# Performance work log

Hardware: AMD Instinct MI355X
Metric: run time of the kernel (lower is better)

Reference implementation:

```python
import jax, jax.numpy as jnp
import numpy as np


def setup_inputs() -> dict:
    key = jax.random.key(0)
    k1, k2, k3, k4, k5 = jax.random.split(key, 5)
    B, H, W, C = 4, 64, 64, 512
    ratio = 8
    d = C // ratio  # 64
    x = jax.random.normal(k1, (B, H, W, C), dtype=jnp.float32)
    # 1x1 conv weights (no bias) == channel-mixing matrices, he_normal-ish scale
    Wq = jax.random.normal(k2, (C, d), dtype=jnp.float32) * np.sqrt(2.0 / C)
    Wk = jax.random.normal(k3, (C, d), dtype=jnp.float32) * np.sqrt(2.0 / C)
    Wv = jax.random.normal(k4, (C, C), dtype=jnp.float32) * np.sqrt(2.0 / C)
    gamma = jax.random.normal(k5, (1,), dtype=jnp.float32)
    return {"x": x, "Wq": Wq, "Wk": Wk, "Wv": Wv, "gamma": gamma}


def reference(x, Wq, Wk, Wv, gamma):
    B, H, W, C = x.shape
    N = H * W
    # 1x1 convs (no bias) are per-pixel channel matmuls
    q = jnp.einsum('bhwc,cd->bhwd', x, Wq).reshape(B, N, -1)  # [B,N,d]
    k = jnp.einsum('bhwc,cd->bhwd', x, Wk).reshape(B, N, -1)  # [B,N,d]
    v = jnp.einsum('bhwc,cd->bhwd', x, Wv).reshape(B, N, C)   # [B,N,C]
    # energy[b,i,j] = key_i . query_j  (batch_dot(key, query^T))
    energy = jnp.einsum('bid,bjd->bij', k, q)                 # [B,N,N]
    attn = jax.nn.softmax(energy, axis=-1)
    out = jnp.einsum('bij,bjc->bic', attn, v)                 # [B,N,C]
    out = out.reshape(B, H, W, C)
    return gamma * out
```

## Files before the change

### kernel.cpp

```cpp
#include <hip/hip_runtime.h>
#include <hip/hip_bf16.h>

typedef unsigned short u16;
typedef unsigned int   u32;
typedef __attribute__((ext_vector_type(8))) short short8;
typedef __attribute__((ext_vector_type(4))) float f32x4;
typedef __attribute__((ext_vector_type(4))) u16   u16x4;

#define MFMA16(a,b,c) __builtin_amdgcn_mfma_f32_16x16x32_bf16((a),(b),(c),0,0,0)

#define BATCH 4
#define NPIX  4096
#define CCH   512
#define DDIM  64
#define MFIX  64.0f

static __device__ __forceinline__ u16 f2bf(float f){
  __hip_bfloat16 h = __float2bfloat16(f);
  return __builtin_bit_cast(u16, h);
}
static __device__ __forceinline__ float bf2f(u16 u){
  __hip_bfloat16 h = __builtin_bit_cast(__hip_bfloat16, u);
  return __bfloat162float(h);
}

__global__ __launch_bounds__(256) void k_wconv(const f32x4* __restrict__ wv,
                                               u16x4* __restrict__ wvb){
  const int i = blockIdx.x*256 + threadIdx.x;
  #pragma unroll
  for (int it=0; it<4; ++it){
    int idx = i + it*16384;
    f32x4 v = wv[idx];
    u16x4 o;
    o[0]=f2bf(v[0]); o[1]=f2bf(v[1]); o[2]=f2bf(v[2]); o[3]=f2bf(v[3]);
    wvb[idx] = o;
  }
}

__global__ __launch_bounds__(256) void k_qkproj(const float* __restrict__ x,
                                                const float* __restrict__ Wq,
                                                const float* __restrict__ Wk,
                                                u16* __restrict__ qhi, u16* __restrict__ qlo,
                                                u16* __restrict__ khi, u16* __restrict__ klo,
                                                u16* __restrict__ xhi){
  __shared__ float xs[32][512];
  const int pix0 = blockIdx.x * 32;
  {
    const f32x4* xg = (const f32x4*)(x + (size_t)pix0*CCH);
    f32x4* xsv = (f32x4*)(&xs[0][0]);
    #pragma unroll
    for (int it=0; it<16; ++it) xsv[threadIdx.x + it*256] = xg[threadIdx.x + it*256];
  }
  __syncthreads();
  #pragma unroll
  for (int e=0; e<16; ++e){
    int idx4 = e*256 + threadIdx.x;
    int f = idx4*4;
    int row = f >> 9, col = f & 511;
    f32x4 v = *(const f32x4*)(&xs[row][col]);
    u16x4 o;
    o[0]=f2bf(v[0]); o[1]=f2bf(v[1]); o[2]=f2bf(v[2]); o[3]=f2bf(v[3]);
    *(u16x4*)(&xhi[(size_t)(pix0+row)*CCH + col]) = o;
  }
  const int col = threadIdx.x & 127;
  const int grp = threadIdx.x >> 7;
  const float* W = (col < 64) ? Wq : Wk;
  const int wc = col & 63;
  float acc[16];
  #pragma unroll
  for (int p=0;p<16;++p) acc[p] = 0.f;
  #pragma unroll 2
  for (int c=0;c<512;c+=4){
    float w0 = W[(c+0)*64 + wc];
    float w1 = W[(c+1)*64 + wc];
    float w2 = W[(c+2)*64 + wc];
    float w3 = W[(c+3)*64 + wc];
    #pragma unroll
    for (int p=0;p<16;++p){
      f32x4 xv = *(const f32x4*)(&xs[grp*16+p][c]);
      acc[p] += xv[0]*w0 + xv[1]*w1 + xv[2]*w2 + xv[3]*w3;
    }
  }
  #pragma unroll
  for (int p=0;p<16;++p){
    int pix = pix0 + grp*16 + p;
    float v = acc[p];
    u16 hi = f2bf(v);
    u16 lo = f2bf(v - bf2f(hi));
    if (col < 64){ qhi[pix*64+wc] = hi; qlo[pix*64+wc] = lo; }
    else         { khi[pix*64+wc] = hi; klo[pix*64+wc] = lo; }
  }
}

__global__ __launch_bounds__(256) void k_vproj(const u16* __restrict__ xhi,
                                               const u16* __restrict__ wvb,
                                               u16* __restrict__ vJB){
  __shared__ u16 As[64][72];
  __shared__ u16 Bs[64][266];
  const int pix0 = blockIdx.x * 64;
  const int c0   = blockIdx.y * 256;
  const int tid = threadIdx.x;
  const int w = tid >> 6, l = tid & 63;
  const int lg = l >> 4, ll = l & 15;
  f32x4 acc[4][4];
  #pragma unroll
  for (int mf=0;mf<4;++mf)
    #pragma unroll
    for (int nf=0;nf<4;++nf){ f32x4 z = {0.f,0.f,0.f,0.f}; acc[mf][nf] = z; }

  for (int ks=0; ks<8; ++ks){
    __syncthreads();
    #pragma unroll
    for (int it=0; it<2; ++it){
      int ch = tid + it*256; int r = ch>>3, c8 = ch&7;
      *(uint4*)(&As[r][c8*8]) = *(const uint4*)(&xhi[(size_t)(pix0+r)*CCH + ks*64 + c8*8]);
    }
    #pragma unroll
    for (int it=0; it<8; ++it){
      int ch = tid + it*256; int r = ch>>5, c32 = ch&31;
      uint4 d = *(const uint4*)(&wvb[(size_t)(ks*64+r)*CCH + c0 + c32*8]);
      u32* dst = (u32*)(&Bs[r][c32*8]);
      dst[0]=d.x; dst[1]=d.y; dst[2]=d.z; dst[3]=d.w;
    }
    __syncthreads();
    #pragma unroll
    for (int kc=0;kc<2;++kc){
      short8 a[4];
      #pragma unroll
      for (int mf=0;mf<4;++mf) a[mf] = *(const short8*)(&As[mf*16 + ll][kc*32 + lg*8]);
      #pragma unroll
      for (int nf=0;nf<4;++nf){
        short8 bb;
        int cc = w*64 + nf*16 + ll;
        #pragma unroll
        for (int e=0;e<8;++e) bb[e] = (short)Bs[kc*32 + lg*8 + e][cc];
        #pragma unroll
        for (int mf=0;mf<4;++mf) acc[mf][nf] = MFMA16(a[mf], bb, acc[mf][nf]);
      }
    }
  }
  #pragma unroll
  for (int mf=0;mf<4;++mf){
    #pragma unroll
    for (int nf=0;nf<4;++nf){
      int pix = pix0 + mf*16 + lg*4;
      int c   = c0 + w*64 + nf*16 + ll;
      int bb  = pix >> 12;
      int j   = pix & 4095;
      u16x4 o;
      #pragma unroll
      for (int r=0;r<4;++r) o[r] = f2bf(acc[mf][nf][r]);
      size_t off = (((size_t)bb*64 + (j>>6))*CCH + c)*64 + (j&63);
      *(u16x4*)(vJB + off) = o;
    }
  }
}

__global__ __launch_bounds__(1024,4)
void k_attn(const u16* __restrict__ qhi, const u16* __restrict__ qlo,
            const u16* __restrict__ khi, const u16* __restrict__ klo,
            const u16* __restrict__ vJB, const float* __restrict__ gamma_p,
            float* __restrict__ out){
  __shared__ u16 Qs[2][2][64][76];
  __shared__ u16 Ps[2][64][76];
  __shared__ float l_part[16][16];
  __shared__ float l_s[64];
  const int bid = blockIdx.x;
  const int b  = bid & 3;
  const int i0 = (bid >> 2) * 64;
  const int tid = threadIdx.x;
  const int w = tid >> 6, l = tid & 63;
  const int lg = l >> 4, ll = l & 15;
  const int iw = (w & 3) * 16;
  const int jq = (w >> 2) * 16;
  const int cw = w * 32;

  const u16* qh_b  = qhi + (size_t)b*NPIX*DDIM;
  const u16* ql_b  = qlo + (size_t)b*NPIX*DDIM;
  const u16* vbase = vJB + (size_t)b*64*CCH*64;

  short8 kfh[2], kfl[2];
  #pragma unroll
  for (int kc=0;kc<2;++kc){
    size_t a = ((size_t)(b*NPIX + i0 + iw + ll))*DDIM + kc*32 + lg*8;
    kfh[kc] = *(const short8*)(khi + a);
    kfl[kc] = *(const short8*)(klo + a);
  }

  f32x4 acc[4][2];
  #pragma unroll
  for (int mf=0;mf<4;++mf)
    #pragma unroll
    for (int nf=0;nf<2;++nf){ f32x4 z = {0.f,0.f,0.f,0.f}; acc[mf][nf] = z; }
  float lsum = 0.f;

  const int spart = tid >> 9;
  const int srow  = (tid >> 3) & 63;
  const int sq    = tid & 7;
  const u16* sgl  = spart ? ql_b : qh_b;
  uint4 qr;
  auto stage_load = [&](int j0){
    qr = *(const uint4*)(sgl + (size_t)(j0 + srow)*DDIM + sq*8);
  };
  auto stage_write = [&](int buf){
    *(uint4*)(&Qs[buf][spart][srow][sq*8]) = qr;
  };

  auto s_step = [&](int u){
    const int buf = u & 1;
    f32x4 s = {0.f,0.f,0.f,0.f};
    #pragma unroll
    for (int kc=0;kc<2;++kc){
      short8 qh = *(const short8*)(&Qs[buf][0][jq + ll][kc*32 + lg*8]);
      short8 ql = *(const short8*)(&Qs[buf][1][jq + ll][kc*32 + lg*8]);
      s = MFMA16(qh, kfh[kc], s);
      s = MFMA16(ql, kfh[kc], s);
      s = MFMA16(qh, kfl[kc], s);
    }
    u16x4 pk;
    #pragma unroll
    for (int r=0;r<4;++r){
      float p = __expf(s[r] - MFIX);
      lsum += p;
      pk[r] = f2bf(p);
    }
    *(u16x4*)(&Ps[buf][iw + ll][jq + lg*4]) = pk;
  };

  stage_load(0);    stage_write(0);
  stage_load(64);   stage_write(1);
  stage_load(128);
  __syncthreads();
  s_step(0);

  for (int t=0; t<64; ++t){
    const u16* vt = vbase + (size_t)t*CCH*64;
    short8 vb[4];
    #pragma unroll
    for (int kc=0;kc<2;++kc)
      #pragma unroll
      for (int nf=0;nf<2;++nf)
        vb[kc*2+nf] = *(const short8*)(vt + (size_t)(cw + nf*16 + ll)*64 + kc*32 + lg*8);

    __syncthreads();
    if (t < 62) stage_write(t & 1);
    if (t < 61) stage_load((t+3) * 64);
    if (t < 63) s_step(t + 1);

    #pragma unroll
    for (int kc=0;kc<2;++kc){
      short8 pa[4];
      #pragma unroll
      for (int mf=0;mf<4;++mf) pa[mf] = *(const short8*)(&Ps[t&1][mf*16 + ll][kc*32 + lg*8]);
      #pragma unroll
      for (int nf=0;nf<2;++nf)
        #pragma unroll
        for (int mf=0;mf<4;++mf) acc[mf][nf] = MFMA16(pa[mf], vb[kc*2+nf], acc[mf][nf]);
    }
  }

  lsum += __shfl_xor(lsum, 16);
  lsum += __shfl_xor(lsum, 32);
  if (lg == 0) l_part[w][ll] = lsum;
  __syncthreads();
  if (w < 4 && lg == 0)
    l_s[iw + ll] = (l_part[w][ll]     + l_part[w + 4][ll])
                 + (l_part[w + 8][ll] + l_part[w + 12][ll]);
  __syncthreads();

  const float gm = gamma_p[0];
  #pragma unroll
  for (int mf=0;mf<4;++mf){
    f32x4 inv;
    #pragma unroll
    for (int r=0;r<4;++r) inv[r] = gm / l_s[mf*16 + lg*4 + r];
    #pragma unroll
    for (int nf=0;nf<2;++nf)
      #pragma unroll
      for (int r=0;r<4;++r){
        int row = i0 + mf*16 + lg*4 + r;
        int c   = cw + nf*16 + ll;
        out[((size_t)(b*NPIX + row))*CCH + c] = acc[mf][nf][r] * inv[r];
      }
  }
}

extern "C" void kernel_launch(void* const* d_in, const int* in_sizes, int n_in,
                              void* d_out, int out_size, void* d_ws, size_t ws_size,
                              hipStream_t stream) {
  (void)in_sizes; (void)n_in; (void)out_size; (void)ws_size;
  const float* x  = (const float*)d_in[0];
  const float* Wq = (const float*)d_in[1];
  const float* Wk = (const float*)d_in[2];
  const float* Wv = (const float*)d_in[3];
  const float* gm = (const float*)d_in[4];
  float* out = (float*)d_out;

  u16* qhi = (u16*)d_ws;
  u16* qlo = qhi + (size_t)BATCH*NPIX*DDIM;
  u16* khi = qlo + (size_t)BATCH*NPIX*DDIM;
  u16* klo = khi + (size_t)BATCH*NPIX*DDIM;
  u16* vJB = klo + (size_t)BATCH*NPIX*DDIM;

  u16* xhi = (u16*)d_out;
  u16* wvb = xhi + (size_t)BATCH*NPIX*CCH;

  k_qkproj<<<dim3(512), dim3(256), 0, stream>>>(x, Wq, Wk, qhi, qlo, khi, klo, xhi);
  k_wconv<<<dim3(64), dim3(256), 0, stream>>>((const f32x4*)Wv, (u16x4*)wvb);
  k_vproj<<<dim3(256,2), dim3(256), 0, stream>>>(xhi, wvb, vJB);
  k_attn<<<dim3(256), dim3(1024), 0, stream>>>(qhi, qlo, khi, klo, vJB, gm, out);
}
```

Baseline: 223.7 us.

## Pre-swizzle Q into MFMA fragment layout and load directly into registers

The projection kernel now writes Q hi/lo parts in an MFMA-fragment-ordered layout, so the attention kernel loads each wave's Q operands straight from global memory into registers. This removes the shared-memory Q staging buffer and its LDS traffic. Register double-buffering of the Q fragments replaces the old stage_load/stage_write pipeline. The trade-off is extra register pressure and global loads that each wave issues itself, possibly redundant across waves that share the same q index.

```diff
diff --git a/kernel.cpp b/kernel.cpp
--- a/kernel.cpp
+++ b/kernel.cpp
@@ -14,6 +14,7 @@
 #define CCH   512
 #define DDIM  64
 #define MFIX  64.0f
+#define QF_B  524288
 
 static __device__ __forceinline__ u16 f2bf(float f){
   __hip_bfloat16 h = __float2bfloat16(f);
@@ -40,7 +41,7 @@
 __global__ __launch_bounds__(256) void k_qkproj(const float* __restrict__ x,
                                                 const float* __restrict__ Wq,
                                                 const float* __restrict__ Wk,
-                                                u16* __restrict__ qhi, u16* __restrict__ qlo,
+                                                u16* __restrict__ qf,
                                                 u16* __restrict__ khi, u16* __restrict__ klo,
                                                 u16* __restrict__ xhi){
   __shared__ float xs[32][512];
@@ -87,8 +88,16 @@
     float v = acc[p];
     u16 hi = f2bf(v);
     u16 lo = f2bf(v - bf2f(hi));
-    if (col < 64){ qhi[pix*64+wc] = hi; qlo[pix*64+wc] = lo; }
-    else         { khi[pix*64+wc] = hi; klo[pix*64+wc] = lo; }
+    if (col < 64){
+      int bq = pix >> 12, j = pix & 4095;
+      size_t off = ((size_t)((((j>>6)*4 + ((j>>4)&3))*2 + 0)*2 + (wc>>5)) << 9)
+                 + (size_t)((((j&15) | (((wc>>3)&3)<<4)) << 3) + (wc&7))
+                 + (size_t)bq*QF_B;
+      qf[off]        = hi;
+      qf[off + 1024] = lo;
+    } else {
+      khi[pix*64+wc] = hi; klo[pix*64+wc] = lo;
+    }
   }
 }
 
@@ -157,11 +166,10 @@
 }
 
 __global__ __launch_bounds__(1024,4)
-void k_attn(const u16* __restrict__ qhi, const u16* __restrict__ qlo,
+void k_attn(const u16* __restrict__ qf,
             const u16* __restrict__ khi, const u16* __restrict__ klo,
             const u16* __restrict__ vJB, const float* __restrict__ gamma_p,
             float* __restrict__ out){
-  __shared__ u16 Qs[2][2][64][76];
   __shared__ u16 Ps[2][64][76];
   __shared__ float l_part[16][16];
   __shared__ float l_s[64];
@@ -172,11 +180,10 @@
   const int w = tid >> 6, l = tid & 63;
   const int lg = l >> 4, ll = l & 15;
   const int iw = (w & 3) * 16;
-  const int jq = (w >> 2) * 16;
+  const int q  = w >> 2;
   const int cw = w * 32;
 
-  const u16* qh_b  = qhi + (size_t)b*NPIX*DDIM;
-  const u16* ql_b  = qlo + (size_t)b*NPIX*DDIM;
+  const u16* qf_b  = qf  + (size_t)b*QF_B;
   const u16* vbase = vJB + (size_t)b*64*CCH*64;
 
   short8 kfh[2], kfl[2];
@@ -194,29 +201,31 @@
     for (int nf=0;nf<2;++nf){ f32x4 z = {0.f,0.f,0.f,0.f}; acc[mf][nf] = z; }
   float lsum = 0.f;
 
-  const int spart = tid >> 9;
-  const int srow  = (tid >> 3) & 63;
-  const int sq    = tid & 7;
-  const u16* sgl  = spart ? ql_b : qh_b;
-  uint4 qr;
-  auto stage_load = [&](int j0){
-    qr = *(const uint4*)(sgl + (size_t)(j0 + srow)*DDIM + sq*8);
-  };
-  auto stage_write = [&](int buf){
-    *(uint4*)(&Qs[buf][spart][srow][sq*8]) = qr;
-  };
-
-  auto s_step = [&](int u){
+  auto qf_load = [&](int u, short8 (&dst)[4]){
+    const u16* p = qf_b + ((size_t)(u*4 + q) << 11) + l*8;
+    dst[0] = *(const short8*)(p);
+    dst[1] = *(const short8*)(p + 512);
+    dst[2] = *(const short8*)(p + 1024);
+    dst[3] = *(const short8*)(p + 1536);
+  };
+  auto vb_load = [&](int t, short8 (&dst)[4]){
+    const u16* vt = vbase + (size_t)t*CCH*64;
+    #pragma unroll
+    for (int kc=0;kc<2;++kc)
+      #pragma unroll
+      for (int nf=0;nf<2;++nf)
+        dst[kc*2+nf] = *(const short8*)(vt + (size_t)(cw + nf*16 + ll)*64 + kc*32 + lg*8);
+  };
+
+  auto s_step = [&](int u, short8 (&qfr)[4]){
     const int buf = u & 1;
     f32x4 s = {0.f,0.f,0.f,0.f};
-    #pragma unroll
-    for (int kc=0;kc<2;++kc){
-      short8 qh = *(const short8*)(&Qs[buf][0][jq + ll][kc*32 + lg*8]);
-      short8 ql = *(const short8*)(&Qs[buf][1][jq + ll][kc*32 + lg*8]);
-      s = MFMA16(qh, kfh[kc], s);
-      s = MFMA16(ql, kfh[kc], s);
-      s = MFMA16(qh, kfl[kc], s);
-    }
+    s = MFMA16(qfr[0], kfh[0], s);
+    s = MFMA16(qfr[1], kfh[1], s);
+    s = MFMA16(qfr[2], kfh[0], s);
+    s = MFMA16(qfr[3], kfh[1], s);
+    s = MFMA16(qfr[0], kfl[0], s);
+    s = MFMA16(qfr[1], kfl[1], s);
     u16x4 pk;
     #pragma unroll
     for (int r=0;r<4;++r){
@@ -224,29 +233,10 @@
       lsum += p;
       pk[r] = f2bf(p);
     }
-    *(u16x4*)(&Ps[buf][iw + ll][jq + lg*4]) = pk;
-  };
-
-  stage_load(0);    stage_write(0);
-  stage_load(64);   stage_write(1);
-  stage_load(128);
-  __syncthreads();
-  s_step(0);
-
-  for (int t=0; t<64; ++t){
-    const u16* vt = vbase + (size_t)t*CCH*64;
-    short8 vb[4];
-    #pragma unroll
-    for (int kc=0;kc<2;++kc)
-      #pragma unroll
-      for (int nf=0;nf<2;++nf)
-        vb[kc*2+nf] = *(const short8*)(vt + (size_t)(cw + nf*16 + ll)*64 + kc*32 + lg*8);
-
-    __syncthreads();
-    if (t < 62) stage_write(t & 1);
-    if (t < 61) stage_load((t+3) * 64);
-    if (t < 63) s_step(t + 1);
-
+    *(u16x4*)(&Ps[buf][iw + ll][q*16 + lg*4]) = pk;
+  };
+
+  auto pv = [&](int t, short8 (&vbr)[4]){
     #pragma unroll
     for (int kc=0;kc<2;++kc){
       short8 pa[4];
@@ -255,8 +245,25 @@
       #pragma unroll
       for (int nf=0;nf<2;++nf)
         #pragma unroll
-        for (int mf=0;mf<4;++mf) acc[mf][nf] = MFMA16(pa[mf], vb[kc*2+nf], acc[mf][nf]);
-    }
+        for (int mf=0;mf<4;++mf) acc[mf][nf] = MFMA16(pa[mf], vbr[kc*2+nf], acc[mf][nf]);
+    }
+  };
+
+  short8 qfA[4], qfB[4], vbr[4];
+  qf_load(0, qfA);
+  qf_load(1, qfB);
+  s_step(0, qfA);
+
+  auto body = [&](int t, short8 (&qfCur)[4], short8 (&qfNxt)[4]){
+    __syncthreads();
+    if (t < 62) qf_load(t+2, qfNxt);
+    vb_load(t, vbr);
+    if (t < 63) s_step(t + 1, qfCur);
+    pv(t, vbr);
+  };
+  for (int tt=0; tt<32; ++tt){
+    body(2*tt,     qfB, qfA);
+    body(2*tt + 1, qfA, qfB);
   }
 
   lsum += __shfl_xor(lsum, 16);
@@ -296,17 +303,16 @@
   const float* gm = (const float*)d_in[4];
   float* out = (float*)d_out;
 
-  u16* qhi = (u16*)d_ws;
-  u16* qlo = qhi + (size_t)BATCH*NPIX*DDIM;
-  u16* khi = qlo + (size_t)BATCH*NPIX*DDIM;
+  u16* qf  = (u16*)d_ws;
+  u16* khi = qf  + (size_t)BATCH*QF_B;
   u16* klo = khi + (size_t)BATCH*NPIX*DDIM;
   u16* vJB = klo + (size_t)BATCH*NPIX*DDIM;
 
   u16* xhi = (u16*)d_out;
   u16* wvb = xhi + (size_t)BATCH*NPIX*CCH;
 
-  k_qkproj<<<dim3(512), dim3(256), 0, stream>>>(x, Wq, Wk, qhi, qlo, khi, klo, xhi);
+  k_qkproj<<<dim3(512), dim3(256), 0, stream>>>(x, Wq, Wk, qf, khi, klo, xhi);
   k_wconv<<<dim3(64), dim3(256), 0, stream>>>((const f32x4*)Wv, (u16x4*)wvb);
   k_vproj<<<dim3(256,2), dim3(256), 0, stream>>>(xhi, wvb, vJB);
-  k_attn<<<dim3(256), dim3(1024), 0, stream>>>(qhi, qlo, khi, klo, vJB, gm, out);
-}
+  k_attn<<<dim3(256), dim3(1024), 0, stream>>>(qf, khi, klo, vJB, gm, out);
+}
```

After: 249.3 us. 1.11x slower.
